# Performance work log

Hardware: AMD Instinct MI355X
Metric: run time of the kernel (lower is better)

The kernel has to match this reference:

```python
import jax, jax.numpy as jnp
import numpy as np

DIM, HEADS, DHEAD, CTX_DIM, FF_MULT = 320, 8, 40, 768, 4
INNER_FF = FF_MULT * DIM  # 1280
EPS = 1e-5


def layer_norm(x, g, b):
    mu = jnp.mean(x, axis=-1, keepdims=True)
    var = jnp.mean((x - mu) ** 2, axis=-1, keepdims=True)
    return (x - mu) * jax.lax.rsqrt(var + EPS) * g + b


def attention(x, ctx, wq, wk, wv, wo, bo):
    # x: [b, i, DIM], ctx: [b, j, c]
    b, i, _ = x.shape
    j = ctx.shape[1]
    q = (x @ wq).reshape(b, i, HEADS, DHEAD)
    k = (ctx @ wk).reshape(b, j, HEADS, DHEAD)
    v = (ctx @ wv).reshape(b, j, HEADS, DHEAD)
    scale = DHEAD ** -0.5
    sim = jnp.einsum('bihd,bjhd->bhij', q, k) * scale  # full NxN, non-flash
    attn = jax.nn.softmax(sim, axis=-1)
    out = jnp.einsum('bhij,bjhd->bihd', attn, v).reshape(b, i, HEADS * DHEAD)
    return out @ wo + bo


def setup_inputs() -> dict:
    key = jax.random.key(0)
    ks = jax.random.split(key, 24)
    nrm = lambda k, shp, fan: jax.random.normal(k, shp, jnp.float32) * (fan ** -0.5)
    d = {
        'x': jax.random.normal(ks[0], (1, 4096, DIM), jnp.float32),
        'context': jax.random.normal(ks[1], (1, 77, CTX_DIM), jnp.float32),
        'n1_g': jnp.ones((DIM,), jnp.float32), 'n1_b': jnp.zeros((DIM,), jnp.float32),
        'a1_wq': nrm(ks[2], (DIM, DIM), DIM), 'a1_wk': nrm(ks[3], (DIM, DIM), DIM),
        'a1_wv': nrm(ks[4], (DIM, DIM), DIM), 'a1_wo': nrm(ks[5], (DIM, DIM), DIM),
        'a1_bo': jnp.zeros((DIM,), jnp.float32),
        'n2_g': jnp.ones((DIM,), jnp.float32), 'n2_b': jnp.zeros((DIM,), jnp.float32),
        'a2_wq': nrm(ks[6], (DIM, DIM), DIM), 'a2_wk': nrm(ks[7], (CTX_DIM, DIM), CTX_DIM),
        'a2_wv': nrm(ks[8], (CTX_DIM, DIM), CTX_DIM), 'a2_wo': nrm(ks[9], (DIM, DIM), DIM),
        'a2_bo': jnp.zeros((DIM,), jnp.float32),
        'n3_g': jnp.ones((DIM,), jnp.float32), 'n3_b': jnp.zeros((DIM,), jnp.float32),
        'ff_w1': nrm(ks[10], (DIM, 2 * INNER_FF), DIM),
        'ff_b1': jnp.zeros((2 * INNER_FF,), jnp.float32),
        'ff_w2': nrm(ks[11], (INNER_FF, DIM), INNER_FF),
        'ff_b2': jnp.zeros((DIM,), jnp.float32),
    }
    return d


def reference(x, context, n1_g, n1_b, a1_wq, a1_wk, a1_wv, a1_wo, a1_bo,
              n2_g, n2_b, a2_wq, a2_wk, a2_wv, a2_wo, a2_bo,
              n3_g, n3_b, ff_w1, ff_b1, ff_w2, ff_b2):
    # self-attention
    x = attention(layer_norm(x, n1_g, n1_b), layer_norm(x, n1_g, n1_b),
                  a1_wq, a1_wk, a1_wv, a1_wo, a1_bo) + x
    # cross-attention with text context
    x = attention(layer_norm(x, n2_g, n2_b), context,
                  a2_wq, a2_wk, a2_wv, a2_wo, a2_bo) + x
    # GEGLU feed-forward
    h = layer_norm(x, n3_g, n3_b) @ ff_w1 + ff_b1
    val, gate = jnp.split(h, 2, axis=-1)
    x = (val * jax.nn.gelu(gate, approximate=False)) @ ff_w2 + ff_b2 + x
    return x
```

## Files before the change

kernel.cpp:

```cpp
#include <hip/hip_runtime.h>
#include <hip/hip_bf16.h>
#include <math.h>

typedef __bf16 bf16;
typedef __attribute__((ext_vector_type(8))) __bf16 bf16x8;
typedef __attribute__((ext_vector_type(4))) __bf16 bf16x4;
typedef __attribute__((ext_vector_type(4))) float f32x4;
typedef __attribute__((ext_vector_type(2))) float f32x2;
typedef __attribute__((ext_vector_type(4))) short shortx4;

#define NTOK 4096
#define DIM  320
#define HEADS 8
#define DHEAD 40
#define NCTX 77
#define CTXD 768
#define IFF  1280

#define QSCALE (0.15811388300841897f * 1.4426950408889634f)

__device__ __forceinline__ bf16x8 bzero8() {
    bf16x8 v;
#pragma unroll
    for (int e = 0; e < 8; ++e) v[e] = (bf16)0.0f;
    return v;
}

__device__ __forceinline__ void gld_lds16(const void* g, void* l) {
    __builtin_amdgcn_global_load_lds(
        (const __attribute__((address_space(1))) void*)g,
        (__attribute__((address_space(3))) void*)l, 16, 0, 0);
}

template <int NJ>
struct TJobs { const float* s[NJ]; bf16* d[NJ]; };

template <int NJ, int PERM>
__global__ __launch_bounds__(256)
void transpose_multi(TJobs<NJ> jobs, int K, int N) {
    __shared__ float tile[32][33];
    const float* W = jobs.s[blockIdx.z];
    bf16* Wt = jobs.d[blockIdx.z];
    int n0 = blockIdx.x * 32, k0 = blockIdx.y * 32;
    int tx = threadIdx.x, ty = threadIdx.y;
#pragma unroll
    for (int i = 0; i < 4; ++i)
        tile[ty + i * 8][tx] = W[(size_t)(k0 + ty + i * 8) * N + n0 + tx];
    __syncthreads();
#pragma unroll
    for (int i = 0; i < 4; ++i) {
        int n = n0 + ty + i * 8;
        int nd = PERM ? ((n < 1280) ? 2 * n : 2 * (n - 1280) + 1) : n;
        Wt[(size_t)nd * K + k0 + tx] = (bf16)tile[tx][ty + i * 8];
    }
}

__global__ void f32_to_bf16(const float* __restrict__ X, bf16* __restrict__ Y, int n) {
    int i = blockIdx.x * 256 + threadIdx.x;
    if (i < n) Y[i] = (bf16)X[i];
}

__global__ __launch_bounds__(256)
void layernorm_kernel(const float* __restrict__ X, const float* __restrict__ g,
                      const float* __restrict__ b, bf16* __restrict__ Y) {
    int w = threadIdx.x >> 6, lane = threadIdx.x & 63;
    int row = blockIdx.x * 4 + w;
    const float* xr = X + (size_t)row * DIM;
    float v[5];
    float sum = 0.f;
#pragma unroll
    for (int c = 0; c < 5; ++c) { v[c] = xr[c * 64 + lane]; sum += v[c]; }
#pragma unroll
    for (int off = 1; off < 64; off <<= 1) sum += __shfl_xor(sum, off);
    float mu = sum * (1.f / 320.f);
    float vs = 0.f;
#pragma unroll
    for (int c = 0; c < 5; ++c) { float d = v[c] - mu; vs += d * d; }
#pragma unroll
    for (int off = 1; off < 64; off <<= 1) vs += __shfl_xor(vs, off);
    float rs = rsqrtf(vs * (1.f / 320.f) + 1e-5f);
    bf16* yr = Y + (size_t)row * DIM;
#pragma unroll
    for (int c = 0; c < 5; ++c)
        yr[c * 64 + lane] = (bf16)((v[c] - mu) * rs * g[c * 64 + lane] + b[c * 64 + lane]);
}

template <int EPI, int BM>
__global__ __launch_bounds__(256)
void gemm_tb(const bf16* __restrict__ A, const bf16* __restrict__ Bt,
             int M, int N, int K,
             bf16* __restrict__ Y0, bf16* __restrict__ Y1, bf16* __restrict__ Y2,
             float* Yf, const float* __restrict__ bias, const float* res, int trs) {
    constexpr int ABYTES = BM * 128;
    constexpr int ACH = BM / 32;
    constexpr int WM = BM / 2;
    constexpr int MI = WM / 16;
    __shared__ char smem[ABYTES + 8192];
    const int t = threadIdx.x;
    const int lane = t & 63;
    const int w = t >> 6;
    const int wr = w >> 1, wc = w & 1;
    const int m0 = blockIdx.x * BM;
    const int n0 = blockIdx.y * 64;

    f32x4 acc[MI][2];
#pragma unroll
    for (int mi = 0; mi < MI; ++mi)
#pragma unroll
        for (int ni = 0; ni < 2; ++ni)
#pragma unroll
            for (int r = 0; r < 4; ++r) acc[mi][ni][r] = 0.f;

    for (int k0 = 0; k0 < K; k0 += 64) {
#pragma unroll
        for (int i = 0; i < ACH; ++i) {
            int ch = i * 256 + w * 64 + lane;
            int row = ch >> 3, cpos = ch & 7;
            int seg = cpos ^ (row & 7);
            gld_lds16(A + (size_t)(m0 + row) * K + k0 + seg * 8,
                      smem + (size_t)(i * 256 + w * 64) * 16);
        }
#pragma unroll
        for (int i = 0; i < 2; ++i) {
            int ch = i * 256 + w * 64 + lane;
            int row = ch >> 3, cpos = ch & 7;
            int seg = cpos ^ (row & 7);
            gld_lds16(Bt + (size_t)(n0 + row) * K + k0 + seg * 8,
                      smem + ABYTES + (size_t)(i * 256 + w * 64) * 16);
        }
        __syncthreads();

        bf16x8 a[MI][2], bfr[2][2];
#pragma unroll
        for (int mi = 0; mi < MI; ++mi)
#pragma unroll
            for (int kh = 0; kh < 2; ++kh) {
                int row = wr * WM + mi * 16 + (lane & 15);
                a[mi][kh] = *(const bf16x8*)(smem + row * 128 +
                             ((kh * 64 + (lane >> 4) * 16) ^ ((row & 7) << 4)));
            }
#pragma unroll
        for (int ni = 0; ni < 2; ++ni)
#pragma unroll
            for (int kh = 0; kh < 2; ++kh) {
                int row = wc * 32 + ni * 16 + (lane & 15);
                bfr[ni][kh] = *(const bf16x8*)(smem + ABYTES + row * 128 +
                               ((kh * 64 + (lane >> 4) * 16) ^ ((row & 7) << 4)));
            }
#pragma unroll
        for (int mi = 0; mi < MI; ++mi)
#pragma unroll
            for (int ni = 0; ni < 2; ++ni) {
                acc[mi][ni] = __builtin_amdgcn_mfma_f32_16x16x32_bf16(a[mi][0], bfr[ni][0], acc[mi][ni], 0, 0, 0);
                acc[mi][ni] = __builtin_amdgcn_mfma_f32_16x16x32_bf16(a[mi][1], bfr[ni][1], acc[mi][ni], 0, 0, 0);
            }
        __syncthreads();
    }

#pragma unroll
    for (int mi = 0; mi < MI; ++mi)
#pragma unroll
        for (int ni = 0; ni < 2; ++ni) {
            const int col = n0 + wc * 32 + ni * 16 + (lane & 15);
            const int rowb = m0 + wr * WM + mi * 16 + (lane >> 4) * 4;
            if (EPI == 5) {
                if (col < 320) {
#pragma unroll
                    for (int r = 0; r < 4; ++r)
                        Y0[(size_t)(rowb + r) * 320 + col] = (bf16)(acc[mi][ni][r] * QSCALE);
                } else if (col < 640) {
#pragma unroll
                    for (int r = 0; r < 4; ++r)
                        Y1[(size_t)(rowb + r) * 320 + (col - 320)] = (bf16)acc[mi][ni][r];
                } else {
                    bf16x4 tv;
#pragma unroll
                    for (int r = 0; r < 4; ++r) tv[r] = (bf16)acc[mi][ni][r];
                    *(bf16x4*)(Y2 + (size_t)(col - 640) * trs + rowb) = tv;
                }
            } else if (EPI == 7) {
                int bidx = (col & 1) ? (1280 + (col >> 1)) : (col >> 1);
                float bc = bias[bidx];
#pragma unroll
                for (int r = 0; r < 4; ++r) {
                    float v = acc[mi][ni][r] + bc;
                    float other = __shfl_xor(v, 1);
                    if (!(col & 1)) {
                        float gl = 0.5f * other * (1.f + erff(other * 0.70710678118654752f));
                        Y0[(size_t)(rowb + r) * 1280 + (col >> 1)] = (bf16)(v * gl);
                    }
                }
            } else {
#pragma unroll
                for (int r = 0; r < 4; ++r) {
                    int row = rowb + r;
                    if (row < M) {
                        float v = acc[mi][ni][r];
                        if (EPI == 4) Y0[(size_t)row * N + col] = (bf16)(v * QSCALE);
                        else Yf[(size_t)row * N + col] = v + bias[col] + res[(size_t)row * N + col];
                    }
                }
            }
        }
}

__global__ __launch_bounds__(256)
void gemm_small6(const bf16* __restrict__ A, const bf16* __restrict__ Bt,
                 int M, int N, int K,
                 bf16* __restrict__ Y0, bf16* __restrict__ Y2, int trs) {
    __shared__ char smem[24 * 1024];
    const int t = threadIdx.x;
    const int lane = t & 63;
    const int w = t >> 6;
    const int wr = w >> 1, wc = w & 1;
    const int m0 = 0;
    const int n0 = blockIdx.y * 64;

    f32x4 acc[4][2];
#pragma unroll
    for (int mi = 0; mi < 4; ++mi)
#pragma unroll
        for (int ni = 0; ni < 2; ++ni)
#pragma unroll
            for (int r = 0; r < 4; ++r) acc[mi][ni][r] = 0.f;

    for (int k0 = 0; k0 < K; k0 += 64) {
#pragma unroll
        for (int i = 0; i < 4; ++i) {
            int c = t + i * 256;
            int row = c >> 3, seg = c & 7;
            int gr = m0 + row;
            bf16x8 v = bzero8();
            if (gr < M) v = *(const bf16x8*)(A + (size_t)gr * K + k0 + seg * 8);
            *(bf16x8*)(smem + row * 128 + ((seg * 16) ^ ((row & 7) << 4))) = v;
        }
#pragma unroll
        for (int i = 0; i < 2; ++i) {
            int c = t + i * 256;
            int row = c >> 3, seg = c & 7;
            bf16x8 v = *(const bf16x8*)(Bt + (size_t)(n0 + row) * K + k0 + seg * 8);
            *(bf16x8*)(smem + 16 * 1024 + row * 128 + ((seg * 16) ^ ((row & 7) << 4))) = v;
        }
        __syncthreads();

        bf16x8 a[4][2], bfr[2][2];
#pragma unroll
        for (int mi = 0; mi < 4; ++mi)
#pragma unroll
            for (int kh = 0; kh < 2; ++kh) {
                int row = wr * 64 + mi * 16 + (lane & 15);
                a[mi][kh] = *(const bf16x8*)(smem + row * 128 +
                             ((kh * 64 + (lane >> 4) * 16) ^ ((row & 7) << 4)));
            }
#pragma unroll
        for (int ni = 0; ni < 2; ++ni)
#pragma unroll
            for (int kh = 0; kh < 2; ++kh) {
                int row = wc * 32 + ni * 16 + (lane & 15);
                bfr[ni][kh] = *(const bf16x8*)(smem + 16 * 1024 + row * 128 +
                               ((kh * 64 + (lane >> 4) * 16) ^ ((row & 7) << 4)));
            }
#pragma unroll
        for (int mi = 0; mi < 4; ++mi)
#pragma unroll
            for (int ni = 0; ni < 2; ++ni) {
                acc[mi][ni] = __builtin_amdgcn_mfma_f32_16x16x32_bf16(a[mi][0], bfr[ni][0], acc[mi][ni], 0, 0, 0);
                acc[mi][ni] = __builtin_amdgcn_mfma_f32_16x16x32_bf16(a[mi][1], bfr[ni][1], acc[mi][ni], 0, 0, 0);
            }
        __syncthreads();
    }

#pragma unroll
    for (int mi = 0; mi < 4; ++mi)
#pragma unroll
        for (int ni = 0; ni < 2; ++ni) {
            const int col = n0 + wc * 32 + ni * 16 + (lane & 15);
            const int rowb = m0 + wr * 64 + mi * 16 + (lane >> 4) * 4;
            if (col < 320) {
#pragma unroll
                for (int r = 0; r < 4; ++r)
                    if (rowb + r < M) Y0[(size_t)(rowb + r) * 320 + col] = (bf16)acc[mi][ni][r];
            } else {
                bf16x4 tv;
#pragma unroll
                for (int r = 0; r < 4; ++r) tv[r] = (bf16)acc[mi][ni][r];
                *(bf16x4*)(Y2 + (size_t)(col - 320) * trs + rowb) = tv;
            }
        }
}

#define KVT 64
#define KBYTES 5120
#define VBYTES 6144
#define FBUF (KBYTES + VBYTES)

template <int DIRECT>
__global__ __launch_bounds__(256, 4)
void flash_attn5(const bf16* __restrict__ Qg, const bf16* __restrict__ Kg,
                 const bf16* __restrict__ VTg, bf16* __restrict__ O,
                 float* __restrict__ Opart, float* __restrict__ MLpart,
                 int nkv, int vstride, int tiles_per_split) {
    __shared__ char smem[2 * FBUF];
    const int t = threadIdx.x, lane = t & 63, w = t >> 6;
    const int g = lane >> 4, q = lane & 15;
    const int h = blockIdx.y, split = blockIdx.z;
    const int qb = blockIdx.x * 64 + w * 16;

    const int ntiles = (nkv + KVT - 1) / KVT;
    const int tt0 = split * tiles_per_split;
    int tt1 = tt0 + tiles_per_split;
    if (tt1 > ntiles) tt1 = ntiles;

    if (t < 128) {
        bf16x8 v = bzero8();
        if (((t & 63) >> 3) == 0) {
#pragma unroll
            for (int e = 0; e < 8; ++e) v[e] = (bf16)1.0f;
        }
        *(bf16x8*)(smem + (t >> 6) * FBUF + KBYTES + 5120 + (t & 63) * 16) = v;
    }

    const int nslot = (w == 3) ? 1 : 3;
    const bf16* srcp[3];
    int dstoff[3], sstep[3];
#pragma unroll
    for (int s = 0; s < 3; ++s) {
        int id = w * 3 + s;
        if (id < 5) {
            int c16 = id * 64 + lane;
            int row = c16 / 5, seg = c16 - row * 5;
            srcp[s] = Kg + (size_t)(tt0 * KVT + row) * DIM + h * DHEAD + seg * 8;
            sstep[s] = KVT * DIM;
            dstoff[s] = id * 1024;
        } else {
            int vv = id - 5;
            int c16 = vv * 64 + lane;
            int row = c16 >> 3, seg = (c16 & 7) ^ (row & 7);
            srcp[s] = VTg + (size_t)(h * DHEAD + row) * vstride + tt0 * KVT + seg * 8;
            sstep[s] = KVT;
            dstoff[s] = KBYTES + vv * 1024;
        }
    }

#define STAGE(BUFOFF)                                                     \
    do {                                                                  \
        _Pragma("unroll")                                                 \
        for (int s = 0; s < 3; ++s) {                                     \
            if (s < nslot) {                                              \
                gld_lds16(srcp[s], smem + (BUFOFF) + dstoff[s]);          \
                srcp[s] += sstep[s];                                      \
            }                                                             \
        }                                                                 \
    } while (0)

    bf16x8 qf0 = *(const bf16x8*)(Qg + (size_t)(qb + q) * DIM + h * DHEAD + g * 8);
    bf16x8 qf1 = bzero8();
    if (g == 0) qf1 = *(const bf16x8*)(Qg + (size_t)(qb + q) * DIM + h * DHEAD + 32);

    f32x4 accO[3];
#pragma unroll
    for (int dt = 0; dt < 3; ++dt)
#pragma unroll
        for (int r = 0; r < 4; ++r) accO[dt][r] = 0.f;
    float m_run = -1e30f;

#define TILE_BODY(KSC, J0)                                                        \
    do {                                                                          \
        const char* Ks_ = (KSC);                                                  \
        const char* Vs_ = Ks_ + KBYTES;                                           \
        f32x4 s4[4];                                                              \
        __builtin_amdgcn_s_setprio(1);                                            \
        _Pragma("unroll")                                                         \
        for (int jt = 0; jt < 4; ++jt) {                                          \
            const char* krow = Ks_ + (jt * 16 + q) * 80;                          \
            bf16x8 kb0 = *(const bf16x8*)(krow + g * 16);                         \
            bf16x8 kb1 = bzero8();                                                \
            if (g == 0) kb1 = *(const bf16x8*)(krow + 64);                        \
            f32x4 z;                                                              \
            _Pragma("unroll") for (int r = 0; r < 4; ++r) z[r] = 0.f;             \
            z = __builtin_amdgcn_mfma_f32_16x16x32_bf16(kb0, qf0, z, 0, 0, 0);    \
            z = __builtin_amdgcn_mfma_f32_16x16x32_bf16(kb1, qf1, z, 0, 0, 0);    \
            s4[jt] = z;                                                           \
        }                                                                         \
        __builtin_amdgcn_s_setprio(0);                                            \
        if ((J0) + KVT > nkv) {                                                   \
            _Pragma("unroll") for (int jt = 0; jt < 4; ++jt)                      \
            _Pragma("unroll") for (int r = 0; r < 4; ++r)                         \
                if ((J0) + jt * 16 + g * 4 + r >= nkv) s4[jt][r] = -1e30f;        \
        }                                                                         \
        f32x4 mvv = s4[0];                                                        \
        _Pragma("unroll") for (int jt = 1; jt < 4; ++jt)                          \
        _Pragma("unroll") for (int r = 0; r < 4; ++r)                             \
            mvv[r] = fmaxf(mvv[r], s4[jt][r]);                                    \
        float mt = fmaxf(fmaxf(mvv[0], mvv[1]), fmaxf(mvv[2], mvv[3]));           \
        mt = fmaxf(mt, __shfl_xor(mt, 16));                                       \
        mt = fmaxf(mt, __shfl_xor(mt, 32));                                       \
        if (!__all(mt <= m_run + 8.f)) {                                          \
            float mnew = fmaxf(m_run, mt);                                        \
            float f = exp2f(m_run - mnew);                                        \
            m_run = mnew;                                                         \
            _Pragma("unroll") for (int dt = 0; dt < 3; ++dt)                      \
            _Pragma("unroll") for (int r = 0; r < 4; ++r) accO[dt][r] *= f;       \
        }                                                                         \
        union PU { bf16x4 hv; shortx4 sv; } pk[4];                                \
        _Pragma("unroll") for (int jt = 0; jt < 4; ++jt) {                        \
            bf16x4 hv;                                                            \
            _Pragma("unroll") for (int r = 0; r < 4; ++r)                         \
                hv[r] = (bf16)exp2f(s4[jt][r] - m_run);                           \
            pk[jt].hv = hv;                                                       \
        }                                                                         \
        __builtin_amdgcn_s_setprio(1);                                            \
        _Pragma("unroll") for (int dt = 0; dt < 3; ++dt) {                        \
            const char* vrow = Vs_ + (dt * 16 + q) * 128;                         \
            _Pragma("unroll") for (int jt = 0; jt < 4; ++jt) {                    \
                shortx4 vb = *(const shortx4*)(vrow +                             \
                               ((jt * 32 + g * 8) ^ ((q & 7) << 4)));             \
                accO[dt] = __builtin_amdgcn_mfma_f32_16x16x16bf16_1k(             \
                               vb, pk[jt].sv, accO[dt], 0, 0, 0);                 \
            }                                                                     \
        }                                                                         \
        __builtin_amdgcn_s_setprio(0);                                            \
        __syncthreads();                                                          \
    } while (0)

    STAGE(0);
    __syncthreads();

    int tt = tt0;
    while (tt < tt1) {
        if (tt + 1 < tt1) STAGE(FBUF);
        TILE_BODY(smem, tt * KVT);
        ++tt;
        if (tt >= tt1) break;
        if (tt + 1 < tt1) STAGE(0);
        TILE_BODY(smem + FBUF, tt * KVT);
        ++tt;
    }
#undef TILE_BODY
#undef STAGE

    float l = __shfl(accO[2][0], 32 + q);

    if (DIRECT) {
        float inv = 1.f / l;
#pragma unroll
        for (int dt = 0; dt < 3; ++dt) {
            if (dt < 2 || g < 2) {
                bf16x4 o;
#pragma unroll
                for (int r = 0; r < 4; ++r) o[r] = (bf16)(accO[dt][r] * inv);
                *(bf16x4*)(O + (size_t)(qb + q) * DIM + h * DHEAD + dt * 16 + g * 4) = o;
            }
        }
    } else {
        size_t rowi = (size_t)(split * HEADS + h) * NTOK + qb + q;
#pragma unroll
        for (int dt = 0; dt < 3; ++dt) {
            if (dt < 2 || g < 2)
                *(f32x4*)(Opart + rowi * 40 + dt * 16 + g * 4) = accO[dt];
        }
        if (g == 2) {
            f32x2 ml;
            ml[0] = m_run; ml[1] = accO[2][0];
            *(f32x2*)(MLpart + rowi * 2) = ml;
        }
    }
}

__global__ __launch_bounds__(256)
void flash_combine2(const float* __restrict__ Opart, const float* __restrict__ MLpart,
                    bf16* __restrict__ O) {
    int idx = blockIdx.x * 256 + threadIdx.x;
    int qi = idx / 40, c = idx - qi * 40;
    int h = c / 5, c8 = c - h * 5;
    size_t r0 = (size_t)h * NTOK + qi;
    size_t r1 = (size_t)(HEADS + h) * NTOK + qi;
    f32x2 ml0 = *(const f32x2*)(MLpart + r0 * 2);
    f32x2 ml1 = *(const f32x2*)(MLpart + r1 * 2);
    float M = fmaxf(ml0[0], ml1[0]);
    float w0 = exp2f(ml0[0] - M), w1 = exp2f(ml1[0] - M);
    float inv = 1.f / (w0 * ml0[1] + w1 * ml1[1]);
    const float* o0 = Opart + r0 * 40 + c8 * 8;
    const float* o1 = Opart + r1 * 40 + c8 * 8;
    bf16x8 ov;
#pragma unroll
    for (int e = 0; e < 8; ++e)
        ov[e] = (bf16)((o0[e] * w0 + o1[e] * w1) * inv);
    *(bf16x8*)(O + (size_t)qi * DIM + h * DHEAD + c8 * 8) = ov;
}

extern "C" void kernel_launch(void* const* d_in, const int* in_sizes, int n_in,
                              void* d_out, int out_size, void* d_ws, size_t ws_size,
                              hipStream_t stream) {
    const float* x     = (const float*)d_in[0];
    const float* ctx   = (const float*)d_in[1];
    const float* n1_g  = (const float*)d_in[2];
    const float* n1_b  = (const float*)d_in[3];
    const float* a1_wq = (const float*)d_in[4];
    const float* a1_wk = (const float*)d_in[5];
    const float* a1_wv = (const float*)d_in[6];
    const float* a1_wo = (const float*)d_in[7];
    const float* a1_bo = (const float*)d_in[8];
    const float* n2_g  = (const float*)d_in[9];
    const float* n2_b  = (const float*)d_in[10];
    const float* a2_wq = (const float*)d_in[11];
    const float* a2_wk = (const float*)d_in[12];
    const float* a2_wv = (const float*)d_in[13];
    const float* a2_wo = (const float*)d_in[14];
    const float* a2_bo = (const float*)d_in[15];
    const float* n3_g  = (const float*)d_in[16];
    const float* n3_b  = (const float*)d_in[17];
    const float* ff_w1 = (const float*)d_in[18];
    const float* ff_b1 = (const float*)d_in[19];
    const float* ff_w2 = (const float*)d_in[20];
    const float* ff_b2 = (const float*)d_in[21];

    char* ws = (char*)d_ws;
    size_t off = 0;
    auto alloc = [&](size_t bytes) -> char* {
        char* p = ws + off;
        off += (bytes + 255) & ~(size_t)255;
        return p;
    };
    bf16* lnbuf  = (bf16*)alloc((size_t)NTOK * DIM * 2);
    bf16* qbuf   = (bf16*)alloc((size_t)NTOK * DIM * 2);
    bf16* kbuf   = (bf16*)alloc((size_t)NTOK * DIM * 2);
    bf16* vtbuf  = (bf16*)alloc((size_t)DIM * NTOK * 2);
    bf16* abuf   = (bf16*)alloc((size_t)NTOK * DIM * 2);
    bf16* hbuf   = (bf16*)alloc((size_t)NTOK * 2 * IFF * 2);
    bf16* gbuf   = (bf16*)alloc((size_t)NTOK * IFF * 2);
    bf16* ctxb   = (bf16*)alloc((size_t)NCTX * CTXD * 2);
    bf16* k2buf  = (bf16*)alloc((size_t)128 * DIM * 2);
    bf16* vt2buf = (bf16*)alloc((size_t)DIM * 128 * 2);
    bf16* wqkvT  = (bf16*)alloc((size_t)960 * DIM * 2);
    bf16* woT    = (bf16*)alloc((size_t)DIM * DIM * 2);
    bf16* q2T    = (bf16*)alloc((size_t)DIM * DIM * 2);
    bf16* wkv2T  = (bf16*)alloc((size_t)640 * CTXD * 2);
    bf16* o2T    = (bf16*)alloc((size_t)DIM * DIM * 2);
    bf16* w1T    = (bf16*)alloc((size_t)2 * IFF * DIM * 2);
    bf16* w2T    = (bf16*)alloc((size_t)IFF * DIM * 2);
    float* out   = (float*)d_out;

    float* Opart  = (float*)hbuf;
    float* MLpart = (float*)gbuf;

    dim3 tb(32, 8);
    {
        TJobs<6> j6;
        j6.s[0] = a1_wq; j6.d[0] = wqkvT;
        j6.s[1] = a1_wk; j6.d[1] = wqkvT + (size_t)320 * 320;
        j6.s[2] = a1_wv; j6.d[2] = wqkvT + (size_t)640 * 320;
        j6.s[3] = a1_wo; j6.d[3] = woT;
        j6.s[4] = a2_wq; j6.d[4] = q2T;
        j6.s[5] = a2_wo; j6.d[5] = o2T;
        transpose_multi<6, 0><<<dim3(10, 10, 6), tb, 0, stream>>>(j6, 320, 320);
        TJobs<2> j2;
        j2.s[0] = a2_wk; j2.d[0] = wkv2T;
        j2.s[1] = a2_wv; j2.d[1] = wkv2T + (size_t)320 * 768;
        transpose_multi<2, 0><<<dim3(10, 24, 2), tb, 0, stream>>>(j2, 768, 320);
        TJobs<1> jw1; jw1.s[0] = ff_w1; jw1.d[0] = w1T;
        transpose_multi<1, 1><<<dim3(80, 10, 1), tb, 0, stream>>>(jw1, 320, 2560);
        TJobs<1> jw2; jw2.s[0] = ff_w2; jw2.d[0] = w2T;
        transpose_multi<1, 0><<<dim3(10, 40, 1), tb, 0, stream>>>(jw2, 1280, 320);
    }
    f32_to_bf16<<<231, 256, 0, stream>>>(ctx, ctxb, NCTX * CTXD);

    layernorm_kernel<<<1024, 256, 0, stream>>>(x, n1_g, n1_b, lnbuf);
    gemm_tb<5, 128><<<dim3(32, 15), 256, 0, stream>>>(lnbuf, wqkvT, NTOK, 960, DIM,
                                                      qbuf, kbuf, vtbuf, nullptr, nullptr, nullptr, NTOK);
    flash_attn5<0><<<dim3(64, 8, 2), 256, 0, stream>>>(qbuf, kbuf, vtbuf, nullptr,
                                                       Opart, MLpart, NTOK, NTOK, 32);
    flash_combine2<<<640, 256, 0, stream>>>(Opart, MLpart, abuf);
    gemm_tb<2, 64><<<dim3(64, 5), 256, 0, stream>>>(abuf, woT, NTOK, DIM, DIM,
                                                    nullptr, nullptr, nullptr, out, a1_bo, x, 0);

    layernorm_kernel<<<1024, 256, 0, stream>>>(out, n2_g, n2_b, lnbuf);
    gemm_tb<4, 64><<<dim3(64, 5), 256, 0, stream>>>(lnbuf, q2T, NTOK, DIM, DIM,
                                                    qbuf, nullptr, nullptr, nullptr, nullptr, nullptr, 0);
    gemm_small6<<<dim3(1, 10), 256, 0, stream>>>(ctxb, wkv2T, NCTX, 640, CTXD,
                                                 k2buf, vt2buf, 128);
    flash_attn5<1><<<dim3(64, 8, 1), 256, 0, stream>>>(qbuf, k2buf, vt2buf, abuf,
                                                       nullptr, nullptr, NCTX, 128, 2);
    gemm_tb<2, 64><<<dim3(64, 5), 256, 0, stream>>>(abuf, o2T, NTOK, DIM, DIM,
                                                    nullptr, nullptr, nullptr, out, a2_bo, out, 0);

    layernorm_kernel<<<1024, 256, 0, stream>>>(out, n3_g, n3_b, lnbuf);
    gemm_tb<7, 128><<<dim3(32, 40), 256, 0, stream>>>(lnbuf, w1T, NTOK, 2 * IFF, DIM,
                                                      gbuf, nullptr, nullptr, nullptr, ff_b1, nullptr, 0);
    gemm_tb<2, 64><<<dim3(64, 5), 256, 0, stream>>>(gbuf, w2T, NTOK, DIM, IFF,
                                                    nullptr, nullptr, nullptr, out, ff_b2, out, 0);
}
```

Measured before the change: 200.7 us.

## Double-buffer GEMM K-tiles and split self-attention KV four ways

GEMM kernels now stage the next K tile into a second LDS buffer while the current tile feeds the MFMAs, and precompute per-thread source pointers. This hides global-to-LDS latency and drops one barrier per iteration, but doubles LDS per block, which may lower occupancy. Self-attention splits keys into four chunks instead of two for more blocks in flight. The combine kernel now merges four partial results, which adds partial-buffer traffic.

```diff
diff --git a/kernel.cpp b/kernel.cpp
--- a/kernel.cpp
+++ b/kernel.cpp
@@ -87,22 +87,36 @@
 
 template <int EPI, int BM>
 __global__ __launch_bounds__(256)
-void gemm_tb(const bf16* __restrict__ A, const bf16* __restrict__ Bt,
+void gemm_db(const bf16* __restrict__ A, const bf16* __restrict__ Bt,
              int M, int N, int K,
              bf16* __restrict__ Y0, bf16* __restrict__ Y1, bf16* __restrict__ Y2,
              float* Yf, const float* __restrict__ bias, const float* res, int trs) {
     constexpr int ABYTES = BM * 128;
-    constexpr int ACH = BM / 32;
+    constexpr int FB = ABYTES + 8192;
     constexpr int WM = BM / 2;
     constexpr int MI = WM / 16;
-    __shared__ char smem[ABYTES + 8192];
-    const int t = threadIdx.x;
-    const int lane = t & 63;
-    const int w = t >> 6;
+    constexpr int ACH = BM / 32;
+    __shared__ char smem[2 * FB];
+    const int t = threadIdx.x, lane = t & 63, w = t >> 6;
     const int wr = w >> 1, wc = w & 1;
     const int m0 = blockIdx.x * BM;
     const int n0 = blockIdx.y * 64;
 
+    const bf16* asrc[ACH];
+    const bf16* bsrc[2];
+#pragma unroll
+    for (int i = 0; i < ACH; ++i) {
+        int ch = i * 256 + t;
+        int row = ch >> 3, seg = (ch & 7) ^ (row & 7);
+        asrc[i] = A + (size_t)(m0 + row) * K + seg * 8;
+    }
+#pragma unroll
+    for (int i = 0; i < 2; ++i) {
+        int ch = i * 256 + t;
+        int row = ch >> 3, seg = (ch & 7) ^ (row & 7);
+        bsrc[i] = Bt + (size_t)(n0 + row) * K + seg * 8;
+    }
+
     f32x4 acc[MI][2];
 #pragma unroll
     for (int mi = 0; mi < MI; ++mi)
@@ -111,32 +125,29 @@
 #pragma unroll
             for (int r = 0; r < 4; ++r) acc[mi][ni][r] = 0.f;
 
+    auto STAGE = [&](char* base, int k0) {
+#pragma unroll
+        for (int i = 0; i < ACH; ++i)
+            gld_lds16(asrc[i] + k0, base + (i * 256 + w * 64) * 16);
+#pragma unroll
+        for (int i = 0; i < 2; ++i)
+            gld_lds16(bsrc[i] + k0, base + ABYTES + (i * 256 + w * 64) * 16);
+    };
+
+    char* cur = smem;
+    char* nxt = smem + FB;
+    STAGE(cur, 0);
+    __syncthreads();
+
     for (int k0 = 0; k0 < K; k0 += 64) {
-#pragma unroll
-        for (int i = 0; i < ACH; ++i) {
-            int ch = i * 256 + w * 64 + lane;
-            int row = ch >> 3, cpos = ch & 7;
-            int seg = cpos ^ (row & 7);
-            gld_lds16(A + (size_t)(m0 + row) * K + k0 + seg * 8,
-                      smem + (size_t)(i * 256 + w * 64) * 16);
-        }
-#pragma unroll
-        for (int i = 0; i < 2; ++i) {
-            int ch = i * 256 + w * 64 + lane;
-            int row = ch >> 3, cpos = ch & 7;
-            int seg = cpos ^ (row & 7);
-            gld_lds16(Bt + (size_t)(n0 + row) * K + k0 + seg * 8,
-                      smem + ABYTES + (size_t)(i * 256 + w * 64) * 16);
-        }
-        __syncthreads();
-
-        bf16x8 a[MI][2], bfr[2][2];
+        if (k0 + 64 < K) STAGE(nxt, k0 + 64);
+        bf16x8 a[MI][2], b[2][2];
 #pragma unroll
         for (int mi = 0; mi < MI; ++mi)
 #pragma unroll
             for (int kh = 0; kh < 2; ++kh) {
                 int row = wr * WM + mi * 16 + (lane & 15);
-                a[mi][kh] = *(const bf16x8*)(smem + row * 128 +
+                a[mi][kh] = *(const bf16x8*)(cur + row * 128 +
                              ((kh * 64 + (lane >> 4) * 16) ^ ((row & 7) << 4)));
             }
 #pragma unroll
@@ -144,17 +155,18 @@
 #pragma unroll
             for (int kh = 0; kh < 2; ++kh) {
                 int row = wc * 32 + ni * 16 + (lane & 15);
-                bfr[ni][kh] = *(const bf16x8*)(smem + ABYTES + row * 128 +
-                               ((kh * 64 + (lane >> 4) * 16) ^ ((row & 7) << 4)));
+                b[ni][kh] = *(const bf16x8*)(cur + ABYTES + row * 128 +
+                             ((kh * 64 + (lane >> 4) * 16) ^ ((row & 7) << 4)));
             }
 #pragma unroll
         for (int mi = 0; mi < MI; ++mi)
 #pragma unroll
             for (int ni = 0; ni < 2; ++ni) {
-                acc[mi][ni] = __builtin_amdgcn_mfma_f32_16x16x32_bf16(a[mi][0], bfr[ni][0], acc[mi][ni], 0, 0, 0);
-                acc[mi][ni] = __builtin_amdgcn_mfma_f32_16x16x32_bf16(a[mi][1], bfr[ni][1], acc[mi][ni], 0, 0, 0);
+                acc[mi][ni] = __builtin_amdgcn_mfma_f32_16x16x32_bf16(a[mi][0], b[ni][0], acc[mi][ni], 0, 0, 0);
+                acc[mi][ni] = __builtin_amdgcn_mfma_f32_16x16x32_bf16(a[mi][1], b[ni][1], acc[mi][ni], 0, 0, 0);
             }
         __syncthreads();
+        char* tmp = cur; cur = nxt; nxt = tmp;
     }
 
 #pragma unroll
@@ -468,24 +480,35 @@
 }
 
 __global__ __launch_bounds__(256)
-void flash_combine2(const float* __restrict__ Opart, const float* __restrict__ MLpart,
-                    bf16* __restrict__ O) {
+void flash_combine(const float* __restrict__ Opart, const float* __restrict__ MLpart,
+                   bf16* __restrict__ O) {
     int idx = blockIdx.x * 256 + threadIdx.x;
     int qi = idx / 40, c = idx - qi * 40;
     int h = c / 5, c8 = c - h * 5;
-    size_t r0 = (size_t)h * NTOK + qi;
-    size_t r1 = (size_t)(HEADS + h) * NTOK + qi;
-    f32x2 ml0 = *(const f32x2*)(MLpart + r0 * 2);
-    f32x2 ml1 = *(const f32x2*)(MLpart + r1 * 2);
-    float M = fmaxf(ml0[0], ml1[0]);
-    float w0 = exp2f(ml0[0] - M), w1 = exp2f(ml1[0] - M);
-    float inv = 1.f / (w0 * ml0[1] + w1 * ml1[1]);
-    const float* o0 = Opart + r0 * 40 + c8 * 8;
-    const float* o1 = Opart + r1 * 40 + c8 * 8;
+    float mv[4], lv[4];
+    float M = -1e30f;
+#pragma unroll
+    for (int s = 0; s < 4; ++s) {
+        f32x2 ml = *(const f32x2*)(MLpart + ((size_t)(s * HEADS + h) * NTOK + qi) * 2);
+        mv[s] = ml[0]; lv[s] = ml[1];
+        M = fmaxf(M, ml[0]);
+    }
+    float wgt[4], denom = 0.f;
+#pragma unroll
+    for (int s = 0; s < 4; ++s) { wgt[s] = exp2f(mv[s] - M); denom += wgt[s] * lv[s]; }
+    float inv = 1.f / denom;
+    float o[8];
+#pragma unroll
+    for (int e = 0; e < 8; ++e) o[e] = 0.f;
+#pragma unroll
+    for (int s = 0; s < 4; ++s) {
+        const float* op = Opart + ((size_t)(s * HEADS + h) * NTOK + qi) * 40 + c8 * 8;
+#pragma unroll
+        for (int e = 0; e < 8; ++e) o[e] += wgt[s] * op[e];
+    }
     bf16x8 ov;
 #pragma unroll
-    for (int e = 0; e < 8; ++e)
-        ov[e] = (bf16)((o0[e] * w0 + o1[e] * w1) * inv);
+    for (int e = 0; e < 8; ++e) ov[e] = (bf16)(o[e] * inv);
     *(bf16x8*)(O + (size_t)qi * DIM + h * DHEAD + c8 * 8) = ov;
 }
 
@@ -566,27 +589,27 @@
     f32_to_bf16<<<231, 256, 0, stream>>>(ctx, ctxb, NCTX * CTXD);
 
     layernorm_kernel<<<1024, 256, 0, stream>>>(x, n1_g, n1_b, lnbuf);
-    gemm_tb<5, 128><<<dim3(32, 15), 256, 0, stream>>>(lnbuf, wqkvT, NTOK, 960, DIM,
+    gemm_db<5, 128><<<dim3(32, 15), 256, 0, stream>>>(lnbuf, wqkvT, NTOK, 960, DIM,
                                                       qbuf, kbuf, vtbuf, nullptr, nullptr, nullptr, NTOK);
-    flash_attn5<0><<<dim3(64, 8, 2), 256, 0, stream>>>(qbuf, kbuf, vtbuf, nullptr,
-                                                       Opart, MLpart, NTOK, NTOK, 32);
-    flash_combine2<<<640, 256, 0, stream>>>(Opart, MLpart, abuf);
-    gemm_tb<2, 64><<<dim3(64, 5), 256, 0, stream>>>(abuf, woT, NTOK, DIM, DIM,
+    flash_attn5<0><<<dim3(64, 8, 4), 256, 0, stream>>>(qbuf, kbuf, vtbuf, nullptr,
+                                                       Opart, MLpart, NTOK, NTOK, 16);
+    flash_combine<<<640, 256, 0, stream>>>(Opart, MLpart, abuf);
+    gemm_db<2, 64><<<dim3(64, 5), 256, 0, stream>>>(abuf, woT, NTOK, DIM, DIM,
                                                     nullptr, nullptr, nullptr, out, a1_bo, x, 0);
 
     layernorm_kernel<<<1024, 256, 0, stream>>>(out, n2_g, n2_b, lnbuf);
-    gemm_tb<4, 64><<<dim3(64, 5), 256, 0, stream>>>(lnbuf, q2T, NTOK, DIM, DIM,
+    gemm_db<4, 64><<<dim3(64, 5), 256, 0, stream>>>(lnbuf, q2T, NTOK, DIM, DIM,
                                                     qbuf, nullptr, nullptr, nullptr, nullptr, nullptr, 0);
     gemm_small6<<<dim3(1, 10), 256, 0, stream>>>(ctxb, wkv2T, NCTX, 640, CTXD,
                                                  k2buf, vt2buf, 128);
     flash_attn5<1><<<dim3(64, 8, 1), 256, 0, stream>>>(qbuf, k2buf, vt2buf, abuf,
                                                        nullptr, nullptr, NCTX, 128, 2);
-    gemm_tb<2, 64><<<dim3(64, 5), 256, 0, stream>>>(abuf, o2T, NTOK, DIM, DIM,
+    gemm_db<2, 64><<<dim3(64, 5), 256, 0, stream>>>(abuf, o2T, NTOK, DIM, DIM,
                                                     nullptr, nullptr, nullptr, out, a2_bo, out, 0);
 
     layernorm_kernel<<<1024, 256, 0, stream>>>(out, n3_g, n3_b, lnbuf);
-    gemm_tb<7, 128><<<dim3(32, 40), 256, 0, stream>>>(lnbuf, w1T, NTOK, 2 * IFF, DIM,
+    gemm_db<7, 128><<<dim3(32, 40), 256, 0, stream>>>(lnbuf, w1T, NTOK, 2 * IFF, DIM,
                                                       gbuf, nullptr, nullptr, nullptr, ff_b1, nullptr, 0);
-    gemm_tb<2, 64><<<dim3(64, 5), 256, 0, stream>>>(gbuf, w2T, NTOK, DIM, IFF,
+    gemm_db<2, 64><<<dim3(64, 5), 256, 0, stream>>>(gbuf, w2T, NTOK, DIM, IFF,
                                                     nullptr, nullptr, nullptr, out, ff_b2, out, 0);
 }
```

New measurement: 197.0 us. About the same (-1.8%).
